# Kernel tuning notes

Measured on AMD Instinct MI355X. Metric: run time of the kernel, lower is better.

Reference implementation:

```python
import jax, jax.numpy as jnp
import numpy as np


def setup_inputs() -> dict:
    key = jax.random.key(0)
    ks = jax.random.split(key, 7)
    B, Nc, Nt = 4, 2048, 2048
    D = 512          # key_size == representation_size
    H, E = 8, 64     # num_heads, head_dim = D // H
    return {
        "keys": jax.random.normal(ks[0], (B, Nc, D), dtype=jnp.float32),
        "values": jax.random.normal(ks[1], (B, Nc, D), dtype=jnp.float32),
        "query": jax.random.normal(ks[2], (B, Nt, D), dtype=jnp.float32),
        "Wk": jax.random.normal(ks[3], (H, D, E), dtype=jnp.float32) * 0.02,
        "Wv": jax.random.normal(ks[4], (H, D, E), dtype=jnp.float32) * 0.02,
        "Wq": jax.random.normal(ks[5], (H, D, E), dtype=jnp.float32) * 0.02,
        "Wout": jax.random.normal(ks[6], (D, D), dtype=jnp.float32) * 0.02,
    }


def reference(keys, values, query, Wk, Wv, Wq, Wout):
    # Batched per-head projections (replaces the per-head Python loop)
    k = jnp.einsum("bnd,hde->bhne", keys, Wk)    # [B,H,Nc,E]
    v = jnp.einsum("bnd,hde->bhne", values, Wv)  # [B,H,Nc,E]
    q = jnp.einsum("bnd,hde->bhne", query, Wq)   # [B,H,Nt,E]
    head_dim = q.shape[-1]
    # NOTE: original scales by head_dim (query.size()[2]), not sqrt(head_dim)
    scores = jnp.einsum("bhqe,bhke->bhqk", q, k) / head_dim
    attn = jax.nn.softmax(scores, axis=-1)
    out = jnp.einsum("bhqk,bhke->bhqe", attn, v)  # [B,H,Nt,E]
    # concat over heads (head-major feature order, matches torch.cat(dim=-1))
    B, H, Nt, E = out.shape
    out = jnp.transpose(out, (0, 2, 1, 3)).reshape(B, Nt, H * E)
    # final Linear (no bias): x @ Wout^T
    return out @ Wout.T
```

## Files before the change

### kernel.cpp

```cpp
#include <hip/hip_runtime.h>

#define B_   4
#define H_   8
#define NSEQ 2048
#define D_   512
#define E_   64

typedef __bf16 bf16x8 __attribute__((ext_vector_type(8)));
typedef float  f32x4  __attribute__((ext_vector_type(4)));

__device__ __forceinline__ unsigned short f2b(float f) {
    __bf16 h = (__bf16)f;
    return __builtin_bit_cast(unsigned short, h);
}
__device__ __forceinline__ bf16x8 ld_frag(const unsigned short* p) {
    return *reinterpret_cast<const bf16x8*>(p);
}
__device__ __forceinline__ void wave_lds_fence() {
    __asm__ __volatile__("s_waitcnt lgkmcnt(0)" ::: "memory");
}
__device__ __forceinline__ void async_copy16(const void* g, const unsigned short* l) {
    __builtin_amdgcn_global_load_lds(
        (const __attribute__((address_space(1))) unsigned int*)g,
        (__attribute__((address_space(3))) unsigned int*)l, 16, 0, 0);
}

__global__ __launch_bounds__(256)
void cast_w_kernel(const float* __restrict__ Wk, const float* __restrict__ Wv,
                   const float* __restrict__ Wq, const float* __restrict__ Wo,
                   unsigned short* __restrict__ okt, unsigned short* __restrict__ ovt,
                   unsigned short* __restrict__ oqt, unsigned short* __restrict__ oo) {
    int idx = blockIdx.x * 256 + threadIdx.x;
    int y = blockIdx.y;
    if (y == 3) { oo[idx] = f2b(Wo[idx]); return; }
    const float* src = y == 0 ? Wk : (y == 1 ? Wv : Wq);
    unsigned short* dst = y == 0 ? okt : (y == 1 ? ovt : oqt);
    float scl = (y == 2) ? 0.015625f : 1.0f;
    int hh = idx >> 15, rem = idx & 32767, d = rem >> 6, e = rem & 63;
    dst[hh * 32768 + e * 512 + d] = f2b(src[idx] * scl);
}

__global__ __launch_bounds__(256, 2)
void proj_gemm(const float* __restrict__ query, const float* __restrict__ keys,
               const float* __restrict__ values,
               const unsigned short* __restrict__ wqt,
               const unsigned short* __restrict__ wkt,
               const unsigned short* __restrict__ wvt,
               unsigned short* __restrict__ qb, unsigned short* __restrict__ kb,
               unsigned short* __restrict__ vtb) {
    const int m0  = blockIdx.x * 128;
    const int no0 = blockIdx.y * 64;
    const int which = blockIdx.z;
    const int tid = threadIdx.x;
    const int wave = tid >> 6, lane = tid & 63;
    const int quad = lane >> 4, l16 = lane & 15;

    const float* X = which == 0 ? query : (which == 1 ? keys : values);
    const unsigned short* W = which == 0 ? wqt : (which == 1 ? wkt : wvt);

    __shared__ unsigned short Ab[2][128][72];
    __shared__ unsigned short Bb[2][64][72];

    const float* Xp = X + (size_t)m0 * D_;
    const unsigned short* Wp = W + (size_t)no0 * D_;

    float4 aF[8]; uint4 bU[2];
    #define PROJ_LOAD(k0)                                                      \
        {   _Pragma("unroll")                                                  \
            for (int i = 0; i < 8; ++i) {                                      \
                int idx = tid + i * 256;                                       \
                aF[i] = *reinterpret_cast<const float4*>(                      \
                    Xp + (size_t)(idx >> 4) * D_ + (k0) + (idx & 15) * 4);     \
            }                                                                  \
            _Pragma("unroll")                                                  \
            for (int i = 0; i < 2; ++i) {                                      \
                int idx = tid + i * 256;                                       \
                bU[i] = *reinterpret_cast<const uint4*>(                       \
                    Wp + (size_t)(idx >> 3) * D_ + (k0) + (idx & 7) * 8);      \
            } }
    #define PROJ_COMMIT(buf)                                                   \
        {   _Pragma("unroll")                                                  \
            for (int i = 0; i < 8; ++i) {                                      \
                int idx = tid + i * 256;                                       \
                ushort4 o = make_ushort4(f2b(aF[i].x), f2b(aF[i].y),           \
                                         f2b(aF[i].z), f2b(aF[i].w));          \
                *reinterpret_cast<ushort4*>(&Ab[buf][idx >> 4][(idx & 15) * 4]) = o; \
            }                                                                  \
            _Pragma("unroll")                                                  \
            for (int i = 0; i < 2; ++i) {                                      \
                int idx = tid + i * 256;                                       \
                *reinterpret_cast<uint4*>(&Bb[buf][idx >> 3][(idx & 7) * 8]) = bU[i]; \
            } }

    PROJ_LOAD(0)
    PROJ_COMMIT(0)
    PROJ_LOAD(64)
    __syncthreads();

    const f32x4 z = {0.f, 0.f, 0.f, 0.f};
    f32x4 acc[2][4];
    #pragma unroll
    for (int i = 0; i < 2; ++i)
        #pragma unroll
        for (int j = 0; j < 4; ++j) acc[i][j] = z;

    for (int kt = 0; kt < 8; ++kt) {
        const int cur = kt & 1;
        #pragma unroll
        for (int kk = 0; kk < 2; ++kk) {
            bf16x8 bfr[4];
            #pragma unroll
            for (int nt = 0; nt < 4; ++nt)
                bfr[nt] = ld_frag(&Bb[cur][nt * 16 + l16][kk * 32 + quad * 8]);
            #pragma unroll
            for (int mt = 0; mt < 2; ++mt) {
                bf16x8 af = ld_frag(&Ab[cur][wave * 32 + mt * 16 + l16][kk * 32 + quad * 8]);
                #pragma unroll
                for (int nt = 0; nt < 4; ++nt)
                    acc[mt][nt] = __builtin_amdgcn_mfma_f32_16x16x32_bf16(
                        af, bfr[nt], acc[mt][nt], 0, 0, 0);
            }
        }
        if (kt < 7) {
            PROJ_COMMIT(1 - cur)
            if (kt + 2 < 8) PROJ_LOAD((kt + 2) * 64)
        }
        __syncthreads();
    }

    if (which != 2) {
        unsigned short (*Os)[72] = reinterpret_cast<unsigned short(*)[72]>(&Ab[0][0][0]);
        #pragma unroll
        for (int mt = 0; mt < 2; ++mt)
            #pragma unroll
            for (int nt = 0; nt < 4; ++nt)
                #pragma unroll
                for (int r = 0; r < 4; ++r)
                    Os[wave * 32 + mt * 16 + quad * 4 + r][nt * 16 + l16] =
                        f2b(acc[mt][nt][r]);
        __syncthreads();
        unsigned short* Y = (which == 0 ? qb : kb);
        #pragma unroll
        for (int i = 0; i < 4; ++i) {
            int idx = tid + i * 256;
            int row = idx >> 3, seg = idx & 7;
            *reinterpret_cast<uint4*>(Y + (size_t)(m0 + row) * D_ + no0 + seg * 8) =
                *reinterpret_cast<const uint4*>(&Os[row][seg * 8]);
        }
    } else {
        unsigned short (*Ot)[136] = reinterpret_cast<unsigned short(*)[136]>(&Ab[0][0][0]);
        #pragma unroll
        for (int mt = 0; mt < 2; ++mt)
            #pragma unroll
            for (int nt = 0; nt < 4; ++nt) {
                ushort4 o = make_ushort4(f2b(acc[mt][nt][0]), f2b(acc[mt][nt][1]),
                                         f2b(acc[mt][nt][2]), f2b(acc[mt][nt][3]));
                *reinterpret_cast<ushort4*>(
                    &Ot[nt * 16 + l16][wave * 32 + mt * 16 + quad * 4]) = o;
            }
        __syncthreads();
        const int b = m0 >> 11, nloc = m0 & 2047;
        #pragma unroll
        for (int i = 0; i < 4; ++i) {
            int idx = tid + i * 256;
            int lhe = idx >> 4, seg = idx & 15;
            int ghe = no0 + lhe;
            *reinterpret_cast<uint4*>(
                vtb + ((size_t)(b * H_ + (ghe >> 6)) * E_ + (ghe & 63)) * NSEQ +
                nloc + seg * 8) =
                *reinterpret_cast<const uint4*>(&Ot[lhe][seg * 8]);
        }
    }
    #undef PROJ_LOAD
    #undef PROJ_COMMIT
}

__global__ __launch_bounds__(256, 4)
void attn_kernel(const unsigned short* __restrict__ qbp,
                 const unsigned short* __restrict__ kbp,
                 const unsigned short* __restrict__ vtbp,
                 unsigned short* __restrict__ aob) {
    const int L = blockIdx.x;
    const int bh = L & 31, qt = L >> 5;
    const int b = bh >> 3, h = bh & 7;
    const int n0 = qt * 64;
    const int tid = threadIdx.x;
    const int wave = tid >> 6, lane = tid & 63;
    const int quad = lane >> 4, l16 = lane & 15;

    __shared__ unsigned short Ks[2][4096];
    __shared__ unsigned short Vs[2][4096];
    __shared__ unsigned short Ps[4096];

    const unsigned short* kbase = kbp + (size_t)(b * NSEQ) * D_ + h * 64;
    const unsigned short* vbase = vtbp + (size_t)(b * H_ + h) * E_ * NSEQ;

    const int swzF = (l16 & 7) << 4;
    const int r8   = lane >> 3;
    const int sg   = lane & 7;
    const int colK = (sg * 16) ^ ((r8 & 7) << 4);

    bf16x8 qf[2];
    #pragma unroll
    for (int kk = 0; kk < 2; ++kk)
        qf[kk] = ld_frag(
            qbp + (size_t)(b * NSEQ + n0 + wave * 16 + l16) * D_ +
            h * 64 + kk * 32 + quad * 8);

    #define ATTN_STAGE(j, buf)                                                 \
        {   _Pragma("unroll")                                                  \
            for (int i = 0; i < 2; ++i) {                                      \
                async_copy16(                                                  \
                    (const char*)(kbase +                                      \
                        (size_t)((j) * 64 + wave * 16 + i * 8 + r8) * D_) + colK, \
                    &Ks[buf][wave * 1024 + i * 512]);                          \
                async_copy16(                                                  \
                    (const char*)(vbase +                                      \
                        (size_t)(wave * 16 + i * 8 + r8) * NSEQ + (j) * 64) + colK, \
                    &Vs[buf][wave * 1024 + i * 512]);                          \
            } }

    ATTN_STAGE(0, 0)
    __syncthreads();

    const f32x4 z = {0.f, 0.f, 0.f, 0.f};
    f32x4 oacc[4] = {z, z, z, z};
    float lacc = 0.f;

    for (int j = 0; j < NSEQ / 64; ++j) {
        const int cur = j & 1;
        if (j + 1 < NSEQ / 64) ATTN_STAGE(j + 1, 1 - cur)

        f32x4 sacc[4] = {z, z, z, z};
        #pragma unroll
        for (int kk = 0; kk < 2; ++kk)
            #pragma unroll
            for (int mg = 0; mg < 4; ++mg) {
                bf16x8 af = ld_frag(&Ks[cur][(mg * 16 + l16) * 64 +
                                             ((((kk * 64 + quad * 16) ^ swzF)) >> 1)]);
                sacc[mg] = __builtin_amdgcn_mfma_f32_16x16x32_bf16(
                    af, qf[kk], sacc[mg], 0, 0, 0);
            }

        {
            float ls = 0.f;
            #pragma unroll
            for (int mg = 0; mg < 4; ++mg) {
                float p0 = __expf(sacc[mg][0]);
                float p1 = __expf(sacc[mg][1]);
                float p2 = __expf(sacc[mg][2]);
                float p3 = __expf(sacc[mg][3]);
                ls += (p0 + p1) + (p2 + p3);
                ushort4 pk = make_ushort4(f2b(p0), f2b(p1), f2b(p2), f2b(p3));
                *reinterpret_cast<ushort4*>(
                    &Ps[(wave * 16 + l16) * 64 +
                        ((((mg * 32 + quad * 8) ^ swzF)) >> 1)]) = pk;
            }
            lacc += ls;
        }
        wave_lds_fence();

        #pragma unroll
        for (int kkv = 0; kkv < 2; ++kkv) {
            bf16x8 pf = ld_frag(&Ps[(wave * 16 + l16) * 64 +
                                    ((((kkv * 64 + quad * 16) ^ swzF)) >> 1)]);
            #pragma unroll
            for (int eg = 0; eg < 4; ++eg) {
                bf16x8 af = ld_frag(&Vs[cur][(eg * 16 + l16) * 64 +
                                             ((((kkv * 64 + quad * 16) ^ swzF)) >> 1)]);
                oacc[eg] = __builtin_amdgcn_mfma_f32_16x16x32_bf16(
                    af, pf, oacc[eg], 0, 0, 0);
            }
        }

        __syncthreads();
    }

    {
        float s = lacc;
        s += __shfl_xor(s, 16);
        s += __shfl_xor(s, 32);
        float li = 1.0f / s;
        unsigned short* op =
            aob + (size_t)(b * NSEQ + n0 + wave * 16 + l16) * D_ + h * 64 + quad * 4;
        #pragma unroll
        for (int eg = 0; eg < 4; ++eg) {
            ushort4 o = make_ushort4(f2b(oacc[eg][0] * li), f2b(oacc[eg][1] * li),
                                     f2b(oacc[eg][2] * li), f2b(oacc[eg][3] * li));
            *reinterpret_cast<ushort4*>(op + eg * 16) = o;
        }
    }
    #undef ATTN_STAGE
}

__global__ __launch_bounds__(256, 2)
void out_gemm(const unsigned short* __restrict__ A,
              const unsigned short* __restrict__ Wo,
              float* __restrict__ Out) {
    const int m0  = blockIdx.x * 128;
    const int no0 = blockIdx.y * 64;
    const int tid = threadIdx.x;
    const int wave = tid >> 6, lane = tid & 63;
    const int quad = lane >> 4, l16 = lane & 15;

    __shared__ unsigned short Ab[2][128][72];
    __shared__ unsigned short Bb[2][64][72];

    const unsigned short* Ap = A + (size_t)m0 * D_;
    const unsigned short* Bp = Wo + (size_t)no0 * D_;

    uint4 aU[4], bU[2];
    #define OUT_LOAD(k0)                                                       \
        {   _Pragma("unroll")                                                  \
            for (int i = 0; i < 4; ++i) {                                      \
                int idx = tid + i * 256;                                       \
                aU[i] = *reinterpret_cast<const uint4*>(                       \
                    Ap + (size_t)(idx >> 3) * D_ + (k0) + (idx & 7) * 8);      \
            }                                                                  \
            _Pragma("unroll")                                                  \
            for (int i = 0; i < 2; ++i) {                                      \
                int idx = tid + i * 256;                                       \
                bU[i] = *reinterpret_cast<const uint4*>(                       \
                    Bp + (size_t)(idx >> 3) * D_ + (k0) + (idx & 7) * 8);      \
            } }
    #define OUT_COMMIT(buf)                                                    \
        {   _Pragma("unroll")                                                  \
            for (int i = 0; i < 4; ++i) {                                      \
                int idx = tid + i * 256;                                       \
                *reinterpret_cast<uint4*>(&Ab[buf][idx >> 3][(idx & 7) * 8]) = aU[i]; \
            }                                                                  \
            _Pragma("unroll")                                                  \
            for (int i = 0; i < 2; ++i) {                                      \
                int idx = tid + i * 256;                                       \
                *reinterpret_cast<uint4*>(&Bb[buf][idx >> 3][(idx & 7) * 8]) = bU[i]; \
            } }

    OUT_LOAD(0)
    OUT_COMMIT(0)
    OUT_LOAD(64)
    __syncthreads();

    const f32x4 z = {0.f, 0.f, 0.f, 0.f};
    f32x4 acc[2][4];
    #pragma unroll
    for (int i = 0; i < 2; ++i)
        #pragma unroll
        for (int j = 0; j < 4; ++j) acc[i][j] = z;

    for (int kt = 0; kt < 8; ++kt) {
        const int cur = kt & 1;
        #pragma unroll
        for (int kk = 0; kk < 2; ++kk) {
            bf16x8 bfr[4];
            #pragma unroll
            for (int nt = 0; nt < 4; ++nt)
                bfr[nt] = ld_frag(&Bb[cur][nt * 16 + l16][kk * 32 + quad * 8]);
            #pragma unroll
            for (int mt = 0; mt < 2; ++mt) {
                bf16x8 af = ld_frag(&Ab[cur][wave * 32 + mt * 16 + l16][kk * 32 + quad * 8]);
                #pragma unroll
                for (int nt = 0; nt < 4; ++nt)
                    acc[mt][nt] = __builtin_amdgcn_mfma_f32_16x16x32_bf16(
                        af, bfr[nt], acc[mt][nt], 0, 0, 0);
            }
        }
        if (kt < 7) {
            OUT_COMMIT(1 - cur)
            if (kt + 2 < 8) OUT_LOAD((kt + 2) * 64)
        }
        __syncthreads();
    }
    #pragma unroll
    for (int mt = 0; mt < 2; ++mt)
        #pragma unroll
        for (int nt = 0; nt < 4; ++nt)
            #pragma unroll
            for (int r = 0; r < 4; ++r)
                Out[(size_t)(m0 + wave * 32 + mt * 16 + quad * 4 + r) * D_ +
                    no0 + nt * 16 + l16] = acc[mt][nt][r];
    #undef OUT_LOAD
    #undef OUT_COMMIT
}

extern "C" void kernel_launch(void* const* d_in, const int* in_sizes, int n_in,
                              void* d_out, int out_size, void* d_ws, size_t ws_size,
                              hipStream_t stream) {
    const float* keys   = (const float*)d_in[0];
    const float* values = (const float*)d_in[1];
    const float* query  = (const float*)d_in[2];
    const float* Wk     = (const float*)d_in[3];
    const float* Wv     = (const float*)d_in[4];
    const float* Wq     = (const float*)d_in[5];
    const float* Wout   = (const float*)d_in[6];
    float* out = (float*)d_out;

    unsigned short* ws16 = (unsigned short*)d_ws;
    const size_t XN = (size_t)B_ * NSEQ * D_;
    const size_t WN = (size_t)H_ * D_ * E_;
    unsigned short* wkt = ws16;
    unsigned short* wvt = wkt + WN;
    unsigned short* wqt = wvt + WN;
    unsigned short* wob = wqt + WN;
    unsigned short* qb  = wob + WN;
    unsigned short* kb  = qb + XN;
    unsigned short* vtb = kb + XN;
    unsigned short* aob = vtb + XN;

    cast_w_kernel<<<dim3(1024, 4), 256, 0, stream>>>(Wk, Wv, Wq, Wout,
                                                     wkt, wvt, wqt, wob);

    proj_gemm<<<dim3(64, 8, 3), 256, 0, stream>>>(
        query, keys, values, wqt, wkt, wvt, qb, kb, vtb);

    attn_kernel<<<dim3(1024), 256, 0, stream>>>(qb, kb, vtb, aob);

    out_gemm<<<dim3(64, 8), 256, 0, stream>>>(aob, wob, out);
}
```

Before: 220.8 us.

## Pre-cast activations to bf16 and use async global-to-LDS swizzled loads in GEMMs

Adds a separate kernel that converts query/keys/values to bf16 up front. The projection and output GEMMs then stage tiles directly into LDS with global_load_lds copies and an XOR swizzle, replacing register staging with padded rows. Occupancy hints are raised to 3 blocks per SM. The cost is an extra full pass over the fp32 inputs plus an extra bf16 write and read, and the value buffer aliases the attention output workspace.

```diff
diff --git a/kernel.cpp b/kernel.cpp
--- a/kernel.cpp
+++ b/kernel.cpp
@@ -40,9 +40,27 @@
     dst[hh * 32768 + e * 512 + d] = f2b(src[idx] * scl);
 }
 
-__global__ __launch_bounds__(256, 2)
-void proj_gemm(const float* __restrict__ query, const float* __restrict__ keys,
-               const float* __restrict__ values,
+__global__ __launch_bounds__(256)
+void xcast_kernel(const float* __restrict__ q, const float* __restrict__ k,
+                  const float* __restrict__ v,
+                  unsigned short* __restrict__ qx, unsigned short* __restrict__ kx,
+                  unsigned short* __restrict__ vx) {
+    const int y = blockIdx.y;
+    const float* src = y == 0 ? q : (y == 1 ? k : v);
+    unsigned short* dst = y == 0 ? qx : (y == 1 ? kx : vx);
+    #pragma unroll
+    for (int i = 0; i < 4; ++i) {
+        int e = blockIdx.x * 4096 + i * 1024 + threadIdx.x * 4;
+        float4 f = *reinterpret_cast<const float4*>(src + e);
+        *reinterpret_cast<ushort4*>(dst + e) =
+            make_ushort4(f2b(f.x), f2b(f.y), f2b(f.z), f2b(f.w));
+    }
+}
+
+__global__ __launch_bounds__(256, 3)
+void proj_gemm(const unsigned short* __restrict__ qx,
+               const unsigned short* __restrict__ kx,
+               const unsigned short* __restrict__ vx,
                const unsigned short* __restrict__ wqt,
                const unsigned short* __restrict__ wkt,
                const unsigned short* __restrict__ wvt,
@@ -55,46 +73,36 @@
     const int wave = tid >> 6, lane = tid & 63;
     const int quad = lane >> 4, l16 = lane & 15;
 
-    const float* X = which == 0 ? query : (which == 1 ? keys : values);
+    const unsigned short* X = which == 0 ? qx : (which == 1 ? kx : vx);
     const unsigned short* W = which == 0 ? wqt : (which == 1 ? wkt : wvt);
 
-    __shared__ unsigned short Ab[2][128][72];
-    __shared__ unsigned short Bb[2][64][72];
-
-    const float* Xp = X + (size_t)m0 * D_;
+    __shared__ unsigned short Ab[2][8192];
+    __shared__ unsigned short Bb[2][4096];
+
+    const unsigned short* Xp = X + (size_t)m0 * D_;
     const unsigned short* Wp = W + (size_t)no0 * D_;
 
-    float4 aF[8]; uint4 bU[2];
-    #define PROJ_LOAD(k0)                                                      \
+    const int swzF = (l16 & 7) << 4;
+    const int r8   = lane >> 3;
+    const int sg   = lane & 7;
+    const int colK = (sg * 16) ^ ((r8 & 7) << 4);
+
+    #define PROJ_STAGE(kt, buf)                                                \
         {   _Pragma("unroll")                                                  \
-            for (int i = 0; i < 8; ++i) {                                      \
-                int idx = tid + i * 256;                                       \
-                aF[i] = *reinterpret_cast<const float4*>(                      \
-                    Xp + (size_t)(idx >> 4) * D_ + (k0) + (idx & 15) * 4);     \
-            }                                                                  \
+            for (int i = 0; i < 4; ++i)                                        \
+                async_copy16(                                                  \
+                    (const char*)(Xp + (size_t)(wave * 32 + i * 8 + r8) * D_ + \
+                                  (kt) * 64) + colK,                           \
+                    &Ab[buf][(wave * 32 + i * 8) * 64]);                       \
             _Pragma("unroll")                                                  \
-            for (int i = 0; i < 2; ++i) {                                      \
-                int idx = tid + i * 256;                                       \
-                bU[i] = *reinterpret_cast<const uint4*>(                       \
-                    Wp + (size_t)(idx >> 3) * D_ + (k0) + (idx & 7) * 8);      \
-            } }
-    #define PROJ_COMMIT(buf)                                                   \
-        {   _Pragma("unroll")                                                  \
-            for (int i = 0; i < 8; ++i) {                                      \
-                int idx = tid + i * 256;                                       \
-                ushort4 o = make_ushort4(f2b(aF[i].x), f2b(aF[i].y),           \
-                                         f2b(aF[i].z), f2b(aF[i].w));          \
-                *reinterpret_cast<ushort4*>(&Ab[buf][idx >> 4][(idx & 15) * 4]) = o; \
-            }                                                                  \
-            _Pragma("unroll")                                                  \
-            for (int i = 0; i < 2; ++i) {                                      \
-                int idx = tid + i * 256;                                       \
-                *reinterpret_cast<uint4*>(&Bb[buf][idx >> 3][(idx & 7) * 8]) = bU[i]; \
-            } }
-
-    PROJ_LOAD(0)
-    PROJ_COMMIT(0)
-    PROJ_LOAD(64)
+            for (int i = 0; i < 2; ++i)                                        \
+                async_copy16(                                                  \
+                    (const char*)(Wp + (size_t)(wave * 16 + i * 8 + r8) * D_ + \
+                                  (kt) * 64) + colK,                           \
+                    &Bb[buf][(wave * 16 + i * 8) * 64]);                       \
+        }
+
+    PROJ_STAGE(0, 0)
     __syncthreads();
 
     const f32x4 z = {0.f, 0.f, 0.f, 0.f};
@@ -106,30 +114,28 @@
 
     for (int kt = 0; kt < 8; ++kt) {
         const int cur = kt & 1;
+        if (kt + 1 < 8) PROJ_STAGE(kt + 1, 1 - cur)
         #pragma unroll
         for (int kk = 0; kk < 2; ++kk) {
+            const int co = ((kk * 64 + quad * 16) ^ swzF) >> 1;
             bf16x8 bfr[4];
             #pragma unroll
             for (int nt = 0; nt < 4; ++nt)
-                bfr[nt] = ld_frag(&Bb[cur][nt * 16 + l16][kk * 32 + quad * 8]);
+                bfr[nt] = ld_frag(&Bb[cur][(nt * 16 + l16) * 64 + co]);
             #pragma unroll
             for (int mt = 0; mt < 2; ++mt) {
-                bf16x8 af = ld_frag(&Ab[cur][wave * 32 + mt * 16 + l16][kk * 32 + quad * 8]);
+                bf16x8 af = ld_frag(&Ab[cur][(wave * 32 + mt * 16 + l16) * 64 + co]);
                 #pragma unroll
                 for (int nt = 0; nt < 4; ++nt)
                     acc[mt][nt] = __builtin_amdgcn_mfma_f32_16x16x32_bf16(
                         af, bfr[nt], acc[mt][nt], 0, 0, 0);
             }
         }
-        if (kt < 7) {
-            PROJ_COMMIT(1 - cur)
-            if (kt + 2 < 8) PROJ_LOAD((kt + 2) * 64)
-        }
         __syncthreads();
     }
 
     if (which != 2) {
-        unsigned short (*Os)[72] = reinterpret_cast<unsigned short(*)[72]>(&Ab[0][0][0]);
+        unsigned short (*Os)[72] = reinterpret_cast<unsigned short(*)[72]>(&Ab[0][0]);
         #pragma unroll
         for (int mt = 0; mt < 2; ++mt)
             #pragma unroll
@@ -148,7 +154,7 @@
                 *reinterpret_cast<const uint4*>(&Os[row][seg * 8]);
         }
     } else {
-        unsigned short (*Ot)[136] = reinterpret_cast<unsigned short(*)[136]>(&Ab[0][0][0]);
+        unsigned short (*Ot)[136] = reinterpret_cast<unsigned short(*)[136]>(&Ab[0][0]);
         #pragma unroll
         for (int mt = 0; mt < 2; ++mt)
             #pragma unroll
@@ -171,8 +177,7 @@
                 *reinterpret_cast<const uint4*>(&Ot[lhe][seg * 8]);
         }
     }
-    #undef PROJ_LOAD
-    #undef PROJ_COMMIT
+    #undef PROJ_STAGE
 }
 
 __global__ __launch_bounds__(256, 4)
@@ -293,7 +298,7 @@
     #undef ATTN_STAGE
 }
 
-__global__ __launch_bounds__(256, 2)
+__global__ __launch_bounds__(256, 3)
 void out_gemm(const unsigned short* __restrict__ A,
               const unsigned short* __restrict__ Wo,
               float* __restrict__ Out) {
@@ -303,41 +308,33 @@
     const int wave = tid >> 6, lane = tid & 63;
     const int quad = lane >> 4, l16 = lane & 15;
 
-    __shared__ unsigned short Ab[2][128][72];
-    __shared__ unsigned short Bb[2][64][72];
+    __shared__ unsigned short Ab[2][8192];
+    __shared__ unsigned short Bb[2][4096];
 
     const unsigned short* Ap = A + (size_t)m0 * D_;
     const unsigned short* Bp = Wo + (size_t)no0 * D_;
 
-    uint4 aU[4], bU[2];
-    #define OUT_LOAD(k0)                                                       \
+    const int swzF = (l16 & 7) << 4;
+    const int r8   = lane >> 3;
+    const int sg   = lane & 7;
+    const int colK = (sg * 16) ^ ((r8 & 7) << 4);
+
+    #define OUT_STAGE(kt, buf)                                                 \
         {   _Pragma("unroll")                                                  \
-            for (int i = 0; i < 4; ++i) {                                      \
-                int idx = tid + i * 256;                                       \
-                aU[i] = *reinterpret_cast<const uint4*>(                       \
-                    Ap + (size_t)(idx >> 3) * D_ + (k0) + (idx & 7) * 8);      \
-            }                                                                  \
+            for (int i = 0; i < 4; ++i)                                        \
+                async_copy16(                                                  \
+                    (const char*)(Ap + (size_t)(wave * 32 + i * 8 + r8) * D_ + \
+                                  (kt) * 64) + colK,                           \
+                    &Ab[buf][(wave * 32 + i * 8) * 64]);                       \
             _Pragma("unroll")                                                  \
-            for (int i = 0; i < 2; ++i) {                                      \
-                int idx = tid + i * 256;                                       \
-                bU[i] = *reinterpret_cast<const uint4*>(                       \
-                    Bp + (size_t)(idx >> 3) * D_ + (k0) + (idx & 7) * 8);      \
-            } }
-    #define OUT_COMMIT(buf)                                                    \
-        {   _Pragma("unroll")                                                  \
-            for (int i = 0; i < 4; ++i) {                                      \
-                int idx = tid + i * 256;                                       \
-                *reinterpret_cast<uint4*>(&Ab[buf][idx >> 3][(idx & 7) * 8]) = aU[i]; \
-            }                                                                  \
-            _Pragma("unroll")                                                  \
-            for (int i = 0; i < 2; ++i) {                                      \
-                int idx = tid + i * 256;                                       \
-                *reinterpret_cast<uint4*>(&Bb[buf][idx >> 3][(idx & 7) * 8]) = bU[i]; \
-            } }
-
-    OUT_LOAD(0)
-    OUT_COMMIT(0)
-    OUT_LOAD(64)
+            for (int i = 0; i < 2; ++i)                                        \
+                async_copy16(                                                  \
+                    (const char*)(Bp + (size_t)(wave * 16 + i * 8 + r8) * D_ + \
+                                  (kt) * 64) + colK,                           \
+                    &Bb[buf][(wave * 16 + i * 8) * 64]);                       \
+        }
+
+    OUT_STAGE(0, 0)
     __syncthreads();
 
     const f32x4 z = {0.f, 0.f, 0.f, 0.f};
@@ -349,25 +346,23 @@
 
     for (int kt = 0; kt < 8; ++kt) {
         const int cur = kt & 1;
+        if (kt + 1 < 8) OUT_STAGE(kt + 1, 1 - cur)
         #pragma unroll
         for (int kk = 0; kk < 2; ++kk) {
+            const int co = ((kk * 64 + quad * 16) ^ swzF) >> 1;
             bf16x8 bfr[4];
             #pragma unroll
             for (int nt = 0; nt < 4; ++nt)
-                bfr[nt] = ld_frag(&Bb[cur][nt * 16 + l16][kk * 32 + quad * 8]);
+                bfr[nt] = ld_frag(&Bb[cur][(nt * 16 + l16) * 64 + co]);
             #pragma unroll
             for (int mt = 0; mt < 2; ++mt) {
-                bf16x8 af = ld_frag(&Ab[cur][wave * 32 + mt * 16 + l16][kk * 32 + quad * 8]);
+                bf16x8 af = ld_frag(&Ab[cur][(wave * 32 + mt * 16 + l16) * 64 + co]);
                 #pragma unroll
                 for (int nt = 0; nt < 4; ++nt)
                     acc[mt][nt] = __builtin_amdgcn_mfma_f32_16x16x32_bf16(
                         af, bfr[nt], acc[mt][nt], 0, 0, 0);
             }
         }
-        if (kt < 7) {
-            OUT_COMMIT(1 - cur)
-            if (kt + 2 < 8) OUT_LOAD((kt + 2) * 64)
-        }
         __syncthreads();
     }
     #pragma unroll
@@ -378,8 +373,7 @@
             for (int r = 0; r < 4; ++r)
                 Out[(size_t)(m0 + wave * 32 + mt * 16 + quad * 4 + r) * D_ +
                     no0 + nt * 16 + l16] = acc[mt][nt][r];
-    #undef OUT_LOAD
-    #undef OUT_COMMIT
+    #undef OUT_STAGE
 }
 
 extern "C" void kernel_launch(void* const* d_in, const int* in_sizes, int n_in,
@@ -405,12 +399,18 @@
     unsigned short* kb  = qb + XN;
     unsigned short* vtb = kb + XN;
     unsigned short* aob = vtb + XN;
+    unsigned short* qx  = aob + XN;
+    unsigned short* kx  = qx + XN;
+    unsigned short* vx  = aob;
 
     cast_w_kernel<<<dim3(1024, 4), 256, 0, stream>>>(Wk, Wv, Wq, Wout,
                                                      wkt, wvt, wqt, wob);
 
+    xcast_kernel<<<dim3(1024, 3), 256, 0, stream>>>(query, keys, values,
+                                                    qx, kx, vx);
+
     proj_gemm<<<dim3(64, 8, 3), 256, 0, stream>>>(
-        query, keys, values, wqt, wkt, wvt, qb, kb, vtb);
+        qx, kx, vx, wqt, wkt, wvt, qb, kb, vtb);
 
     attn_kernel<<<dim3(1024), 256, 0, stream>>>(qb, kb, vtb, aob);
 
```

Result: faster. 190.3 us (-13.8%).
